# Kernel tuning notes

Measured on AMD Instinct MI355X. Metric: run time of the kernel, lower is better.

## Reference

```python
import jax, jax.numpy as jnp
import numpy as np

C = 1.0          # curvature
MIN_NORM = 1e-15
EPS = 1e-7       # atanh clamp for fp32

def _sqnorm(x):
    return jnp.sum(x * x, axis=-1, keepdims=True)

def _norm(x):
    return jnp.sqrt(jnp.maximum(_sqnorm(x), MIN_NORM))

def _atanh(u):
    return jnp.arctanh(jnp.clip(u, -1.0 + EPS, 1.0 - EPS))

def mobius_add(x, y, c):
    x2 = _sqnorm(x); y2 = _sqnorm(y)
    xy = jnp.sum(x * y, axis=-1, keepdims=True)
    num = (1.0 + 2.0 * c * xy + c * y2) * x + (1.0 - c * x2) * y
    den = 1.0 + 2.0 * c * xy + c * c * x2 * y2
    return num / jnp.maximum(den, MIN_NORM)

def logmap0(p, c):
    sc = jnp.sqrt(c)
    pn = _norm(p)
    return p / pn / sc * _atanh(sc * pn)

def logmap(p1, p2, c):
    # tangent vector at p1 pointing to p2 (Poincare ball)
    sub = mobius_add(-p1, p2, c)
    sn = _norm(sub)
    lam = 2.0 / jnp.maximum(1.0 - c * _sqnorm(p1), MIN_NORM)
    sc = jnp.sqrt(c)
    return 2.0 / sc / lam * _atanh(sc * sn) * sub / sn

def expmap(p, u, c):
    un = _norm(u)
    lam = 2.0 / jnp.maximum(1.0 - c * _sqnorm(p), MIN_NORM)
    sc = jnp.sqrt(c)
    second = jnp.tanh(sc * lam * un / 2.0) * u / (sc * un)
    return mobius_add(p, second, c)


def setup_inputs() -> dict:
    key = jax.random.key(0)
    k1, k2, k3 = jax.random.split(key, 3)
    B, N, D = 1, 1024, 128
    # points inside the unit Poincare ball (||x|| ~ 0.23)
    x = jax.random.normal(k1, (B, N, D), jnp.float32) * 0.02
    # sparse-ish dense adjacency mask (0/1 floats)
    adj = (jax.random.uniform(k2, (B, N, N)) < 0.05).astype(jnp.float32)
    # DenseAtt: nn.Linear(2*D, 1) weight (flattened) + bias
    att_w = jax.random.normal(k3, (2 * D,), jnp.float32) * 0.1
    att_b = jnp.zeros((), jnp.float32)
    return {"x": x, "adj": adj, "att_w": att_w, "att_b": att_b}


def reference(x, adj, att_w, att_b):
    B, N, D = x.shape
    x_t = logmap0(x, C)                                   # [B,N,D]
    # DenseAtt: sigmoid(Linear(cat(x_i, x_j))) decomposed as left_i + right_j + b
    left = x_t @ att_w[:D]                                # [B,N]
    right = x_t @ att_w[D:]                               # [B,N]
    att = jax.nn.sigmoid(left[:, :, None] + right[:, None, :] + att_b) * adj  # [B,N,N]
    # pairwise logmap: tangent at x_i of every x_j  -> [B,N,N,D]
    x_local = logmap(x[:, :, None, :], x[:, None, :, :], C)
    support_t = jnp.einsum('bij,bijd->bid', att, x_local)  # [B,N,D]
    return expmap(x, support_t, C)
```

## Files before the change

### kernel.cpp

```cpp
#include <hip/hip_runtime.h>
#include <math.h>


typedef short short4v __attribute__((ext_vector_type(4)));
typedef short short8v __attribute__((ext_vector_type(8)));
typedef float float4v __attribute__((ext_vector_type(4)));

static __device__ __forceinline__ short f2bf(float f) {
    unsigned u = __float_as_uint(f);
    u += 0x7fff + ((u >> 16) & 1);
    return (short)(u >> 16);
}
static __device__ __forceinline__ float rcpf(float x) { return __builtin_amdgcn_rcpf(x); }
static __device__ __forceinline__ short8v ld8(const unsigned short* p) {
    short4v lo = *(const short4v*)p;
    short4v hi = *(const short4v*)(p + 4);
    return (short8v){lo[0],lo[1],lo[2],lo[3],hi[0],hi[1],hi[2],hi[3]};
}
static __device__ __forceinline__ float dot4(float4v a, float4v b) {
    return a[0]*b[0] + a[1]*b[1] + a[2]*b[2] + a[3]*b[3];
}
static __device__ __forceinline__ float atanh_over(float pn) {
    float uu = fminf(pn, 1.f - 1e-7f);
    return 0.5f * __logf((1.f + uu) * rcpf(1.f - uu)) * rcpf(pn);
}

__global__ __launch_bounds__(256) void hyp_stats(
    const float* __restrict__ x, const float* __restrict__ w,
    const float* __restrict__ battp,
    float* __restrict__ st_x2, float* __restrict__ st_L, float* __restrict__ st_R)
{
    int row  = blockIdx.x * 4 + (threadIdx.x >> 6);
    int lane = threadIdx.x & 63;
    const float* xr = x + row * 128;
    float a0 = xr[lane], a1 = xr[lane + 64];
    float x2 = a0 * a0 + a1 * a1;
    float dl = a0 * w[lane]       + a1 * w[lane + 64];
    float dr = a0 * w[lane + 128] + a1 * w[lane + 192];
    for (int m = 1; m < 64; m <<= 1) {
        x2 += __shfl_xor(x2, m);
        dl += __shfl_xor(dl, m);
        dr += __shfl_xor(dr, m);
    }
    if (lane == 0) {
        float pn = sqrtf(fmaxf(x2, 1e-15f));
        float f  = atanh_over(pn);
        st_x2[row] = x2;
        st_L[row]  = f * dl + battp[0];
        st_R[row]  = f * dr;
    }
}

__global__ __launch_bounds__(256, 2) void hyp_main(
    const float* __restrict__ x, const float* __restrict__ adj,
    const float* __restrict__ st_x2, const float* __restrict__ st_L,
    const float* __restrict__ st_R,
    float* __restrict__ Yp, float* __restrict__ Sp2)
{
    __shared__ unsigned short sXI [16 * 132];
    __shared__ unsigned short sXJ [128 * 132];
    __shared__ unsigned short sXJt[128 * 132];
    __shared__ unsigned short sW  [16 * 132];

    const int t    = threadIdx.x;
    const int lane = t & 63;
    const int wave = t >> 6;
    const int n    = lane & 15;
    const int q    = lane >> 4;
    const int i0   = blockIdx.x * 16;
    const int c    = blockIdx.y;
    const int j0   = c * 128;

    const float4v* x4 = (const float4v*)x;

    float x2i4[4], bi4[4], li4[4];
#pragma unroll
    for (int r = 0; r < 4; ++r) {
        int i = i0 + q * 4 + r;
        x2i4[r] = st_x2[i];
        li4[r]  = st_L[i];
    }
    float x2j2[2], rj2[2], adjv[2][4];
#pragma unroll
    for (int jsl = 0; jsl < 2; ++jsl) {
        int j = j0 + (wave * 2 + jsl) * 16 + n;
        x2j2[jsl] = st_x2[j];
        rj2[jsl]  = st_R[j];
#pragma unroll
        for (int r = 0; r < 4; ++r)
            adjv[jsl][r] = adj[(i0 + q * 4 + r) * 1024 + j];
    }
#pragma unroll
    for (int r = 0; r < 4; ++r) bi4[r] = 1.f - x2i4[r];

#pragma unroll
    for (int it = 0; it < 2; ++it) {
        int idx = t + it * 256;
        int r = idx >> 5, cc = idx & 31;
        float4v v = x4[(i0 + r) * 32 + cc];
        short4v h = { f2bf(v[0]), f2bf(v[1]), f2bf(v[2]), f2bf(v[3]) };
        *(short4v*)&sXI[r * 132 + cc * 4] = h;
    }
#pragma unroll
    for (int it = 0; it < 4; ++it) {
        int bid = t + it * 256;
        int jr = ((bid >> 4) & 3) | (((bid >> 6) & 7) << 2);
        int dc = (bid & 15) | (((bid >> 9) & 1) << 4);
        float4v v[4];
#pragma unroll
        for (int e = 0; e < 4; ++e)
            v[e] = x4[(j0 + jr * 4 + e) * 32 + dc];
        short4v h[4];
#pragma unroll
        for (int e = 0; e < 4; ++e) {
            h[e] = (short4v){ f2bf(v[e][0]), f2bf(v[e][1]), f2bf(v[e][2]), f2bf(v[e][3]) };
            *(short4v*)&sXJ[(jr * 4 + e) * 132 + dc * 4] = h[e];
        }
#pragma unroll
        for (int d = 0; d < 4; ++d) {
            short4v ht = (short4v){ h[0][d], h[1][d], h[2][d], h[3][d] };
            *(short4v*)&sXJt[(dc * 4 + d) * 132 + jr * 4] = ht;
        }
    }
    __syncthreads();

    short8v afrag[4];
#pragma unroll
    for (int kk = 0; kk < 4; ++kk)
        afrag[kk] = ld8(&sXI[n * 132 + kk * 32 + q * 8]);

    float Sacc[4] = {0.f, 0.f, 0.f, 0.f};

#pragma unroll
    for (int jsl = 0; jsl < 2; ++jsl) {
        int js = wave * 2 + jsl;
        int jrow = js * 16 + n;
        float4v acc = (float4v){0.f, 0.f, 0.f, 0.f};
#pragma unroll
        for (int kk = 0; kk < 4; ++kk) {
            short8v b = ld8(&sXJ[jrow * 132 + kk * 32 + q * 8]);
            acc = __builtin_amdgcn_mfma_f32_16x16x32_bf16(afrag[kk], b, acc, 0, 0, 0);
        }
        float x2j = x2j2[jsl];
        float rj  = rj2[jsl];
#pragma unroll
        for (int r = 0; r < 4; ++r) {
            float G     = acc[r];
            int   i     = q * 4 + r;
            float alpha = 1.f - 2.f * G + x2j;
            float den   = fmaxf(fmaf(x2i4[r], x2j, 1.f - 2.f * G), 1e-15f);
            float rdn   = rcpf(den);
            float bb    = bi4[r];
            float nn2   = alpha * alpha * x2i4[r] + bb * bb * x2j - 2.f * alpha * bb * G;
            float sn    = sqrtf(fmaxf(nn2 * rdn * rdn, 1e-15f));
            float tt    = atanh_over(sn);
            float z     = li4[r] + rj;
            float sig   = rcpf(1.f + __expf(-z));
            float g     = sig * adjv[jsl][r] * tt * rdn;
            Sacc[r]     = fmaf(g, alpha, Sacc[r]);
            sW[i * 132 + js * 16 + n] = (unsigned short)f2bf(g);
        }
    }
    __syncthreads();

    float4v accB[2];
    accB[0] = (float4v){0.f, 0.f, 0.f, 0.f};
    accB[1] = (float4v){0.f, 0.f, 0.f, 0.f};
#pragma unroll
    for (int nsl = 0; nsl < 2; ++nsl) {
        int ns = wave * 2 + nsl;
#pragma unroll
        for (int kk = 0; kk < 4; ++kk) {
            short8v a = ld8(&sW  [n * 132 + kk * 32 + q * 8]);
            short8v b = ld8(&sXJt[(ns * 16 + n) * 132 + kk * 32 + q * 8]);
            accB[nsl] = __builtin_amdgcn_mfma_f32_16x16x32_bf16(a, b, accB[nsl], 0, 0, 0);
        }
    }

    float* Yc = Yp + c * 131072;
#pragma unroll
    for (int nsl = 0; nsl < 2; ++nsl) {
        int ns = wave * 2 + nsl;
#pragma unroll
        for (int r = 0; r < 4; ++r)
            Yc[(i0 + q * 4 + r) * 128 + ns * 16 + n] = accB[nsl][r];
    }
#pragma unroll
    for (int r = 0; r < 4; ++r)
        Sp2[((c * 1024 + i0 + q * 4 + r) * 4 + wave) * 16 + n] = Sacc[r];
}

__global__ __launch_bounds__(256) void hyp_exp(
    const float* __restrict__ x, const float* __restrict__ Yp,
    const float* __restrict__ Sp2, const float* __restrict__ st_x2,
    float* __restrict__ out)
{
    const int t   = threadIdx.x;
    const int row = blockIdx.x * 8 + (t >> 5);
    const int l32 = t & 31;
    float4v y = (float4v){0.f, 0.f, 0.f, 0.f};
    float S = 0.f;
#pragma unroll
    for (int c = 0; c < 8; ++c) {
        y += *(const float4v*)&Yp[c * 131072 + row * 128 + l32 * 4];
        S += Sp2[(c * 1024 + row) * 64 + l32];
        S += Sp2[(c * 1024 + row) * 64 + 32 + l32];
    }
#pragma unroll
    for (int m = 1; m < 32; m <<= 1) S += __shfl_xor(S, m, 32);

    float4v xa = ((const float4v*)x)[row * 32 + l32];
    float x2 = st_x2[row];
    float bE = fmaxf(1.f - x2, 1e-15f);
    float u[4], un2p = 0.f, xup = 0.f;
#pragma unroll
    for (int e = 0; e < 4; ++e) {
        u[e] = bE * (bE * y[e] - S * xa[e]);
        un2p += u[e] * u[e];
        xup  += xa[e] * u[e];
    }
#pragma unroll
    for (int m = 1; m < 32; m <<= 1) {
        un2p += __shfl_xor(un2p, m, 32);
        xup  += __shfl_xor(xup,  m, 32);
    }
    float un  = sqrtf(fmaxf(un2p, 1e-15f));
    float e2  = __expf(2.f * un * rcpf(bE));
    float th  = 1.f - 2.f * rcpf(e2 + 1.f);
    float s2  = th * rcpf(un);
    float xy  = s2 * xup;
    float y2s = th * th;
    float coef = 1.f + 2.f * xy + y2s;
    float den  = fmaxf(1.f + 2.f * xy + x2 * y2s, 1e-15f);
    float rd   = rcpf(den);
    float4v o = { (coef*xa[0] + bE*s2*u[0])*rd, (coef*xa[1] + bE*s2*u[1])*rd,
                  (coef*xa[2] + bE*s2*u[2])*rd, (coef*xa[3] + bE*s2*u[3])*rd };
    ((float4v*)out)[row * 32 + l32] = o;
}

extern "C" void kernel_launch(void* const* d_in, const int* in_sizes, int n_in,
                              void* d_out, int out_size, void* d_ws, size_t ws_size,
                              hipStream_t stream) {
    const float* x    = (const float*)d_in[0];
    const float* adj  = (const float*)d_in[1];
    const float* w    = (const float*)d_in[2];
    const float* batt = (const float*)d_in[3];
    float* out = (float*)d_out;

    float* Yp    = (float*)d_ws;
    float* Sp2   = Yp + 8 * 131072;
    float* st_x2 = Sp2 + 8 * 1024 * 64;
    float* st_L  = st_x2 + 1024;
    float* st_R  = st_L + 1024;

    hipLaunchKernelGGL(hyp_stats, dim3(256), dim3(256), 0, stream,
                       x, w, batt, st_x2, st_L, st_R);
    hipLaunchKernelGGL(hyp_main, dim3(64, 8), dim3(256), 0, stream,
                       x, adj, st_x2, st_L, st_R, Yp, Sp2);
    hipLaunchKernelGGL(hyp_exp, dim3(128), dim3(256), 0, stream,
                       x, Yp, Sp2, st_x2, out);
}
```

Baseline: 73.87 us.

## Precompute bf16 x and its transpose once, stream into LDS via global_load_lds

The stats kernel now writes bf16 copies of x, both row-major and transposed, with an XOR-swizzled layout. The main kernel fills its LDS tiles with direct global-to-LDS 16-byte loads in place of per-block fp32 loads, bf16 conversion and an in-register transpose. Padded LDS rows are replaced by XOR swizzling, so fragments load as single 16-byte reads. The per-row S partials are now reduced across lanes with shuffles before storage, which shrinks the Sp workspace and the reads in the final kernel. The stats kernel does extra scattered 2-byte writes in exchange.

```diff
diff --git a/kernel.cpp b/kernel.cpp
--- a/kernel.cpp
+++ b/kernel.cpp
@@ -2,7 +2,6 @@
 #include <math.h>
 
 
-typedef short short4v __attribute__((ext_vector_type(4)));
 typedef short short8v __attribute__((ext_vector_type(8)));
 typedef float float4v __attribute__((ext_vector_type(4)));
 
@@ -12,28 +11,37 @@
     return (short)(u >> 16);
 }
 static __device__ __forceinline__ float rcpf(float x) { return __builtin_amdgcn_rcpf(x); }
-static __device__ __forceinline__ short8v ld8(const unsigned short* p) {
-    short4v lo = *(const short4v*)p;
-    short4v hi = *(const short4v*)(p + 4);
-    return (short8v){lo[0],lo[1],lo[2],lo[3],hi[0],hi[1],hi[2],hi[3]};
-}
-static __device__ __forceinline__ float dot4(float4v a, float4v b) {
-    return a[0]*b[0] + a[1]*b[1] + a[2]*b[2] + a[3]*b[3];
-}
 static __device__ __forceinline__ float atanh_over(float pn) {
     float uu = fminf(pn, 1.f - 1e-7f);
     return 0.5f * __logf((1.f + uu) * rcpf(1.f - uu)) * rcpf(pn);
 }
+static __device__ __forceinline__ void gload16(const unsigned short* g, unsigned short* l) {
+    __builtin_amdgcn_global_load_lds(
+        (const __attribute__((address_space(1))) void*)g,
+        (__attribute__((address_space(3))) void*)l, 16, 0, 0);
+}
 
 __global__ __launch_bounds__(256) void hyp_stats(
     const float* __restrict__ x, const float* __restrict__ w,
     const float* __restrict__ battp,
-    float* __restrict__ st_x2, float* __restrict__ st_L, float* __restrict__ st_R)
+    float* __restrict__ st_x2, float* __restrict__ st_L, float* __restrict__ st_R,
+    unsigned short* __restrict__ xb, unsigned short* __restrict__ xbT)
 {
     int row  = blockIdx.x * 4 + (threadIdx.x >> 6);
     int lane = threadIdx.x & 63;
     const float* xr = x + row * 128;
     float a0 = xr[lane], a1 = xr[lane + 64];
+
+    unsigned short b0 = (unsigned short)f2bf(a0);
+    unsigned short b1 = (unsigned short)f2bf(a1);
+    int r7 = row & 7, l7 = lane & 7;
+    xb[row * 128 + ((lane >> 3) ^ r7) * 8 + l7]        = b0;
+    xb[row * 128 + (((lane + 64) >> 3) ^ r7) * 8 + l7] = b1;
+    int tb = (row >> 7) * 128 + (row & 7);
+    int uo = (row & 127) >> 3;
+    xbT[lane * 1024        + tb + (uo ^ l7) * 8] = b0;
+    xbT[(lane + 64) * 1024 + tb + (uo ^ l7) * 8] = b1;
+
     float x2 = a0 * a0 + a1 * a1;
     float dl = a0 * w[lane]       + a1 * w[lane + 64];
     float dr = a0 * w[lane + 128] + a1 * w[lane + 192];
@@ -52,15 +60,16 @@
 }
 
 __global__ __launch_bounds__(256, 2) void hyp_main(
-    const float* __restrict__ x, const float* __restrict__ adj,
+    const float* __restrict__ adj,
     const float* __restrict__ st_x2, const float* __restrict__ st_L,
     const float* __restrict__ st_R,
-    float* __restrict__ Yp, float* __restrict__ Sp2)
+    const unsigned short* __restrict__ xb, const unsigned short* __restrict__ xbT,
+    float* __restrict__ Yp, float* __restrict__ Sp)
 {
-    __shared__ unsigned short sXI [16 * 132];
-    __shared__ unsigned short sXJ [128 * 132];
-    __shared__ unsigned short sXJt[128 * 132];
-    __shared__ unsigned short sW  [16 * 132];
+    __shared__ __align__(16) unsigned short sXI [16 * 128];
+    __shared__ __align__(16) unsigned short sXJ [128 * 128];
+    __shared__ __align__(16) unsigned short sXJt[128 * 128];
+    __shared__ __align__(16) unsigned short sW  [16 * 128];
 
     const int t    = threadIdx.x;
     const int lane = t & 63;
@@ -71,7 +80,16 @@
     const int c    = blockIdx.y;
     const int j0   = c * 128;
 
-    const float4v* x4 = (const float4v*)x;
+    gload16(&xb[i0 * 128 + t * 8], &sXI[wave * 512]);
+#pragma unroll
+    for (int it = 0; it < 8; ++it)
+        gload16(&xb[j0 * 128 + (it * 256 + t) * 8], &sXJ[(it * 256 + wave * 64) * 8]);
+#pragma unroll
+    for (int it = 0; it < 8; ++it) {
+        int s = it * 256 + t;
+        gload16(&xbT[(s >> 4) * 1024 + j0 + (s & 15) * 8],
+                &sXJt[(it * 256 + wave * 64) * 8]);
+    }
 
     float x2i4[4], bi4[4], li4[4];
 #pragma unroll
@@ -93,41 +111,13 @@
 #pragma unroll
     for (int r = 0; r < 4; ++r) bi4[r] = 1.f - x2i4[r];
 
-#pragma unroll
-    for (int it = 0; it < 2; ++it) {
-        int idx = t + it * 256;
-        int r = idx >> 5, cc = idx & 31;
-        float4v v = x4[(i0 + r) * 32 + cc];
-        short4v h = { f2bf(v[0]), f2bf(v[1]), f2bf(v[2]), f2bf(v[3]) };
-        *(short4v*)&sXI[r * 132 + cc * 4] = h;
-    }
-#pragma unroll
-    for (int it = 0; it < 4; ++it) {
-        int bid = t + it * 256;
-        int jr = ((bid >> 4) & 3) | (((bid >> 6) & 7) << 2);
-        int dc = (bid & 15) | (((bid >> 9) & 1) << 4);
-        float4v v[4];
-#pragma unroll
-        for (int e = 0; e < 4; ++e)
-            v[e] = x4[(j0 + jr * 4 + e) * 32 + dc];
-        short4v h[4];
-#pragma unroll
-        for (int e = 0; e < 4; ++e) {
-            h[e] = (short4v){ f2bf(v[e][0]), f2bf(v[e][1]), f2bf(v[e][2]), f2bf(v[e][3]) };
-            *(short4v*)&sXJ[(jr * 4 + e) * 132 + dc * 4] = h[e];
-        }
-#pragma unroll
-        for (int d = 0; d < 4; ++d) {
-            short4v ht = (short4v){ h[0][d], h[1][d], h[2][d], h[3][d] };
-            *(short4v*)&sXJt[(dc * 4 + d) * 132 + jr * 4] = ht;
-        }
-    }
     __syncthreads();
 
+    const int n7 = n & 7;
     short8v afrag[4];
 #pragma unroll
     for (int kk = 0; kk < 4; ++kk)
-        afrag[kk] = ld8(&sXI[n * 132 + kk * 32 + q * 8]);
+        afrag[kk] = *(const short8v*)&sXI[(n * 16 + ((kk * 4 + q) ^ n7)) * 8];
 
     float Sacc[4] = {0.f, 0.f, 0.f, 0.f};
 
@@ -138,7 +128,7 @@
         float4v acc = (float4v){0.f, 0.f, 0.f, 0.f};
 #pragma unroll
         for (int kk = 0; kk < 4; ++kk) {
-            short8v b = ld8(&sXJ[jrow * 132 + kk * 32 + q * 8]);
+            short8v b = *(const short8v*)&sXJ[(jrow * 16 + ((kk * 4 + q) ^ n7)) * 8];
             acc = __builtin_amdgcn_mfma_f32_16x16x32_bf16(afrag[kk], b, acc, 0, 0, 0);
         }
         float x2j = x2j2[jsl];
@@ -158,7 +148,7 @@
             float sig   = rcpf(1.f + __expf(-z));
             float g     = sig * adjv[jsl][r] * tt * rdn;
             Sacc[r]     = fmaf(g, alpha, Sacc[r]);
-            sW[i * 132 + js * 16 + n] = (unsigned short)f2bf(g);
+            sW[(i * 16 + ((js * 2 + (n >> 3)) ^ (i & 7))) * 8 + n7] = (unsigned short)f2bf(g);
         }
     }
     __syncthreads();
@@ -171,8 +161,8 @@
         int ns = wave * 2 + nsl;
 #pragma unroll
         for (int kk = 0; kk < 4; ++kk) {
-            short8v a = ld8(&sW  [n * 132 + kk * 32 + q * 8]);
-            short8v b = ld8(&sXJt[(ns * 16 + n) * 132 + kk * 32 + q * 8]);
+            short8v a = *(const short8v*)&sW  [(n * 16 + ((kk * 4 + q) ^ n7)) * 8];
+            short8v b = *(const short8v*)&sXJt[((ns * 16 + n) * 16 + ((kk * 4 + q) ^ n7)) * 8];
             accB[nsl] = __builtin_amdgcn_mfma_f32_16x16x32_bf16(a, b, accB[nsl], 0, 0, 0);
         }
     }
@@ -186,26 +176,31 @@
             Yc[(i0 + q * 4 + r) * 128 + ns * 16 + n] = accB[nsl][r];
     }
 #pragma unroll
-    for (int r = 0; r < 4; ++r)
-        Sp2[((c * 1024 + i0 + q * 4 + r) * 4 + wave) * 16 + n] = Sacc[r];
+    for (int r = 0; r < 4; ++r) {
+#pragma unroll
+        for (int m = 1; m < 16; m <<= 1)
+            Sacc[r] += __shfl_xor(Sacc[r], m);
+    }
+    if (n == 0) {
+#pragma unroll
+        for (int r = 0; r < 4; ++r)
+            Sp[(c * 1024 + i0 + q * 4 + r) * 4 + wave] = Sacc[r];
+    }
 }
 
 __global__ __launch_bounds__(256) void hyp_exp(
     const float* __restrict__ x, const float* __restrict__ Yp,
-    const float* __restrict__ Sp2, const float* __restrict__ st_x2,
+    const float* __restrict__ Sp, const float* __restrict__ st_x2,
     float* __restrict__ out)
 {
     const int t   = threadIdx.x;
     const int row = blockIdx.x * 8 + (t >> 5);
     const int l32 = t & 31;
     float4v y = (float4v){0.f, 0.f, 0.f, 0.f};
-    float S = 0.f;
-#pragma unroll
-    for (int c = 0; c < 8; ++c) {
+#pragma unroll
+    for (int c = 0; c < 8; ++c)
         y += *(const float4v*)&Yp[c * 131072 + row * 128 + l32 * 4];
-        S += Sp2[(c * 1024 + row) * 64 + l32];
-        S += Sp2[(c * 1024 + row) * 64 + 32 + l32];
-    }
+    float S = Sp[((l32 >> 2) * 1024 + row) * 4 + (l32 & 3)];
 #pragma unroll
     for (int m = 1; m < 32; m <<= 1) S += __shfl_xor(S, m, 32);
 
@@ -248,15 +243,17 @@
     float* out = (float*)d_out;
 
     float* Yp    = (float*)d_ws;
-    float* Sp2   = Yp + 8 * 131072;
-    float* st_x2 = Sp2 + 8 * 1024 * 64;
+    float* Sp    = Yp + 8 * 131072;
+    float* st_x2 = Sp + 8 * 1024 * 4;
     float* st_L  = st_x2 + 1024;
     float* st_R  = st_L + 1024;
+    unsigned short* xb  = (unsigned short*)(st_R + 1024);
+    unsigned short* xbT = xb + 1024 * 128;
 
     hipLaunchKernelGGL(hyp_stats, dim3(256), dim3(256), 0, stream,
-                       x, w, batt, st_x2, st_L, st_R);
+                       x, w, batt, st_x2, st_L, st_R, xb, xbT);
     hipLaunchKernelGGL(hyp_main, dim3(64, 8), dim3(256), 0, stream,
-                       x, adj, st_x2, st_L, st_R, Yp, Sp2);
+                       adj, st_x2, st_L, st_R, xb, xbT, Yp, Sp);
     hipLaunchKernelGGL(hyp_exp, dim3(128), dim3(256), 0, stream,
-                       x, Yp, Sp2, st_x2, out);
-}
+                       x, Yp, Sp, st_x2, out);
+}
```

Result: no change. 72.68 us (median of 2 runs) (-1.6%).
